# Kernel tuning notes

Measured on AMD Instinct MI355X. Metric: run time of the kernel, lower is better.

Reference implementation:

```python
import jax, jax.numpy as jnp
import numpy as np

EPS = 1e-5

def bn_relu(y, g, b):
    # BatchNorm1d in training mode: stats over (B, L) per channel, biased variance
    mu = jnp.mean(y, axis=(0, 2), keepdims=True)
    var = jnp.var(y, axis=(0, 2), keepdims=True)
    yn = (y - mu) * jax.lax.rsqrt(var + EPS)
    return jax.nn.relu(yn * g[None, :, None] + b[None, :, None])

def conv1x1_pad1(x, W):
    # Conv1d(k=1, padding=1, bias=False): pointwise matmul then zero-pad length by 1 each side
    y = jnp.einsum('bcl,oc->bol', x, W)
    return jnp.pad(y, ((0, 0), (0, 0), (1, 1)))

def conv1x1(x, W, b):
    return jnp.einsum('bcl,oc->bol', x, W) + b[None, :, None]

def conv3_pad1(x, W):
    # Conv1d(k=3, padding=1, bias=False); W: [O, C, 3]
    return jax.lax.conv_general_dilated(x, W, window_strides=(1,), padding=((1, 1),),
                                        dimension_numbers=('NCH', 'OIH', 'NCH'))

def pam(f, Wq, bq, Wk, bk, Wv, bv, gamma):
    q = conv1x1(f, Wq, bq)          # [B, C//8, L]
    k = conv1x1(f, Wk, bk)          # [B, C//8, L]
    v = conv1x1(f, Wv, bv)          # [B, C, L]
    energy = jnp.einsum('bql,bqm->blm', q, k)   # [B, L, L]
    attn = jax.nn.softmax(energy, axis=-1)
    out = jnp.einsum('bcm,blm->bcl', v, attn)
    return gamma * out + f

def cam(f, gamma):
    energy = jnp.einsum('bcl,bdl->bcd', f, f)    # [B, C, C]
    energy_new = jnp.max(energy, axis=-1, keepdims=True) - energy
    attn = jax.nn.softmax(energy_new, axis=-1)
    out = jnp.einsum('bcd,bdl->bcl', attn, f)
    return gamma * out + f

def setup_inputs() -> dict:
    key = jax.random.key(0)
    ks = jax.random.split(key, 24)
    B, C, L = 8, 256, 2046
    IC, OC = C // 4, 128  # inter_channels=64, out_channels
    s = 0.05
    d = {
        'x':   jax.random.normal(ks[0], (B, C, L), jnp.float32),
        'W5a': jax.random.normal(ks[1], (IC, C), jnp.float32) * s,
        'g5a': jnp.ones((IC,), jnp.float32), 'b5a': jnp.zeros((IC,), jnp.float32),
        'W5c': jax.random.normal(ks[2], (IC, C), jnp.float32) * s,
        'g5c': jnp.ones((IC,), jnp.float32), 'b5c': jnp.zeros((IC,), jnp.float32),
        'Wq':  jax.random.normal(ks[3], (IC // 8, IC), jnp.float32) * s,
        'bq':  jnp.zeros((IC // 8,), jnp.float32),
        'Wk':  jax.random.normal(ks[4], (IC // 8, IC), jnp.float32) * s,
        'bk':  jnp.zeros((IC // 8,), jnp.float32),
        'Wv':  jax.random.normal(ks[5], (IC, IC), jnp.float32) * s,
        'bv':  jnp.zeros((IC,), jnp.float32),
        'gamma_pam': jnp.full((1,), 0.1, jnp.float32),
        'gamma_cam': jnp.full((1,), 0.1, jnp.float32),
        'W51': jax.random.normal(ks[6], (IC, IC, 3), jnp.float32) * s,
        'g51': jnp.ones((IC,), jnp.float32), 'b51': jnp.zeros((IC,), jnp.float32),
        'W52': jax.random.normal(ks[7], (IC, IC, 3), jnp.float32) * s,
        'g52': jnp.ones((IC,), jnp.float32), 'b52': jnp.zeros((IC,), jnp.float32),
        'W6':  jax.random.normal(ks[8], (OC, IC), jnp.float32) * s,
        'b6':  jnp.zeros((OC,), jnp.float32),
        'W7':  jax.random.normal(ks[9], (OC, IC), jnp.float32) * s,
        'b7':  jnp.zeros((OC,), jnp.float32),
        'W8':  jax.random.normal(ks[10], (OC, IC), jnp.float32) * s,
        'b8':  jnp.zeros((OC,), jnp.float32),
    }
    return d

def reference(x, W5a, g5a, b5a, W5c, g5c, b5c, Wq, bq, Wk, bk, Wv, bv,
              gamma_pam, gamma_cam, W51, g51, b51, W52, g52, b52,
              W6, b6, W7, b7, W8, b8):
    # dropout (p=0.1) treated as identity (eval mode)
    feat1 = bn_relu(conv1x1_pad1(x, W5a), g5a, b5a)          # [B, IC, L+2]
    sa_feat = pam(feat1, Wq, bq, Wk, bk, Wv, bv, gamma_pam)
    sa_conv = bn_relu(conv3_pad1(sa_feat, W51), g51, b51)
    sa_output = conv1x1(sa_conv, W6, b6)                     # [B, OC, L+2]
    feat2 = bn_relu(conv1x1_pad1(x, W5c), g5c, b5c)
    sc_feat = cam(feat2, gamma_cam)
    sc_conv = bn_relu(conv3_pad1(sc_feat, W52), g52, b52)
    sc_output = conv1x1(sc_conv, W7, b7)
    feat_sum = sa_conv + sc_conv
    sasc = conv1x1(feat_sum, W8, b8)
    # pool == 'maxpool' selects AdaptiveAvgPool1d(1) in the original (note swap)
    sasc = jnp.mean(sasc, axis=-1)                            # [B, OC]
    return (sasc, sa_output, sc_output)
```

## Files before the change

### kernel.cpp

```cpp
#include <hip/hip_runtime.h>
#include <math.h>

#define B 8
#define C 256
#define L 2046
#define LP 2048
#define IC 64
#define OC 128
#define BN_EPS 1e-5f
#define INVN (1.f / 16384.f)

#define OFF_Y1T    0u
#define OFF_Y2C    524288u
#define OFF_Y51T   2097152u
#define OFF_Y52T   2621440u
#define OFF_VB     3145728u
#define OFF_QT     3670016u
#define OFF_KT     3735552u
#define OFF_EPART  3866624u
#define OFF_STATS1 4423680u
#define OFF_STATS2 4424704u
#define OFF_W5BF   4425728u
#define OFF_W67    4442112u
#define OFF_WT     4450304u
#define OFF_WQKV   4462592u
#define OFF_BQKV   4465152u

typedef __attribute__((ext_vector_type(8))) short bshort8;
typedef __attribute__((ext_vector_type(4))) float f32x4;

__device__ __forceinline__ unsigned short f2bf(float f) {
    union { float f; unsigned int u; } v; v.f = f;
    return (unsigned short)((v.u + 0x8000u) >> 16);
}
__device__ __forceinline__ float bf2f(unsigned short u) {
    union { unsigned int i; float f; } v; v.i = ((unsigned int)u) << 16;
    return v.f;
}
__device__ __forceinline__ unsigned int pk2(float a, float b) {
    union { float f; unsigned int u; } va, vb; va.f = a; vb.f = b;
    return __builtin_amdgcn_perm(vb.u + 0x8000u, va.u + 0x8000u, 0x07060302u);
}

__device__ __forceinline__ void load_coef(const float* __restrict__ STATS,
        const float* __restrict__ g, const float* __restrict__ beta,
        int base, int cnt, float* cA, float* cB, int t) {
    if (t < cnt) {
        int ch = base + t;
        float s = STATS[ch * 2] + STATS[256 + ch * 2] + STATS[512 + ch * 2] + STATS[768 + ch * 2];
        float q = STATS[ch * 2 + 1] + STATS[256 + ch * 2 + 1] + STATS[512 + ch * 2 + 1] + STATS[768 + ch * 2 + 1];
        float mu = s * INVN;
        float var = q * INVN - mu * mu;
        float A = g[t] * rsqrtf(var + BN_EPS);
        cA[t] = A;
        cB[t] = beta[t] - mu * A;
    }
}

__global__ __launch_bounds__(256) void k_wprep(
        const float* __restrict__ W5a, const float* __restrict__ W5c,
        const float* __restrict__ W6, const float* __restrict__ W7,
        const float* __restrict__ W51, const float* __restrict__ W52,
        const float* __restrict__ Wq, const float* __restrict__ Wk,
        const float* __restrict__ Wv, const float* __restrict__ bq,
        const float* __restrict__ bk, const float* __restrict__ bv,
        const float* __restrict__ b8,
        unsigned short* __restrict__ W5BF, unsigned short* __restrict__ W67,
        unsigned short* __restrict__ WT, unsigned short* __restrict__ WQKV,
        float* __restrict__ BQKV, float* __restrict__ STATS1,
        float* __restrict__ STATS2, float* __restrict__ out_sasc) {
    int i = blockIdx.x * 256 + threadIdx.x;
    if (i < 32768) {
        int o = i >> 8, c = i & 255;
        W5BF[i] = f2bf(o < 64 ? W5a[o * 256 + c] : W5c[(o - 64) * 256 + c]);
    } else if (i < 49152) {
        int j = i - 32768; int g = j >> 13; int r = j & 8191;
        W67[j] = f2bf(g ? W7[r] : W6[r]);
    } else if (i < 73728) {
        int j = i - 49152;
        int c = j & 63, o = (j >> 6) & 63, wt = j >> 12; int w = wt / 3, t = wt % 3;
        const float* Ws = w ? W52 : W51;
        WT[j] = f2bf(Ws[(o * 64 + c) * 3 + t]);
    } else if (i < 78848) {
        int j = i - 73728; int o = j >> 6, c = j & 63;
        float v = o < 8 ? Wq[o * 64 + c] : (o < 16 ? Wk[(o - 8) * 64 + c] : Wv[(o - 16) * 64 + c]);
        WQKV[j] = f2bf(v);
    } else if (i < 78928) {
        int o = i - 78848;
        BQKV[o] = o < 8 ? bq[o] : (o < 16 ? bk[o - 8] : bv[o - 16]);
    } else if (i < 80976) {
        int j = i - 78928;
        if (j < 1024) STATS1[j] = 0.f; else STATS2[j - 1024] = 0.f;
    } else if (i < 82000) {
        int j = i - 80976;
        out_sasc[j] = b8[j & 127];
    }
}

__global__ __launch_bounds__(256) void k_conv1(const float* __restrict__ x,
        const unsigned short* __restrict__ W5BF,
        unsigned short* __restrict__ Y1T, unsigned short* __restrict__ Y2C,
        float* __restrict__ STATS1) {
    __shared__ unsigned short xt[64][264];
    __shared__ float lds_part[4][64];
    int lt = blockIdx.x, b = blockIdx.y;
    int l0 = lt * 64;
    int t = threadIdx.x;
    {
        int j = t & 63, cg = t >> 6;
        int ls = l0 - 1 + j;
        bool ok = (ls >= 0) && (ls < L);
        const float* xs = x + (size_t)(b * C + cg * 64) * L + ls;
        unsigned short* row = &xt[j][cg * 64];
#pragma unroll
        for (int c8 = 0; c8 < 8; ++c8) {
            unsigned int pk[4];
#pragma unroll
            for (int i = 0; i < 4; ++i) {
                float v0 = ok ? xs[(size_t)(c8 * 8 + 2 * i) * L] : 0.f;
                float v1 = ok ? xs[(size_t)(c8 * 8 + 2 * i + 1) * L] : 0.f;
                pk[i] = pk2(v0, v1);
            }
            *(uint4*)(row + c8 * 8) = *(const uint4*)pk;
        }
    }
    __syncthreads();
    int w = t >> 6, lane = t & 63, n = lane & 15, quad = lane >> 4;
    bshort8 wf[2][8];
#pragma unroll
    for (int oi = 0; oi < 2; ++oi)
#pragma unroll
        for (int kt = 0; kt < 8; ++kt)
            wf[oi][kt] = *(const bshort8*)(W5BF + (size_t)((w * 2 + oi) * 16 + n) * C + kt * 32 + quad * 8);
    f32x4 acc[2][4];
#pragma unroll
    for (int oi = 0; oi < 2; ++oi)
#pragma unroll
        for (int sub = 0; sub < 4; ++sub) acc[oi][sub] = (f32x4){0.f, 0.f, 0.f, 0.f};
#pragma unroll
    for (int sub = 0; sub < 4; ++sub) {
        int lloc = sub * 16 + n;
#pragma unroll
        for (int kt = 0; kt < 8; ++kt) {
            bshort8 xb = *(const bshort8*)(&xt[lloc][kt * 32 + quad * 8]);
            acc[0][sub] = __builtin_amdgcn_mfma_f32_16x16x32_bf16(wf[0][kt], xb, acc[0][sub], 0, 0, 0);
            acc[1][sub] = __builtin_amdgcn_mfma_f32_16x16x32_bf16(wf[1][kt], xb, acc[1][sub], 0, 0, 0);
        }
    }
    if (w < 2) {
#pragma unroll
        for (int sub = 0; sub < 4; ++sub) {
            int lp = l0 + sub * 16 + n;
#pragma unroll
            for (int oi = 0; oi < 2; ++oi) {
                int ot = w * 2 + oi;
                uint2 pv;
                pv.x = pk2(acc[oi][sub][0], acc[oi][sub][1]);
                pv.y = pk2(acc[oi][sub][2], acc[oi][sub][3]);
                *(uint2*)(Y1T + ((size_t)(b * LP + lp)) * IC + ot * 16 + quad * 4) = pv;
            }
        }
    } else {
#pragma unroll
        for (int oi = 0; oi < 2; ++oi) {
            int ot = (w - 2) * 2 + oi;
#pragma unroll
            for (int r = 0; r < 4; ++r) {
                int o = ot * 16 + quad * 4 + r;
                unsigned short* dst = Y2C + ((size_t)(b * IC + o)) * LP + l0;
#pragma unroll
                for (int sub = 0; sub < 4; ++sub)
                    dst[sub * 16 + n] = f2bf(acc[oi][sub][r]);
            }
        }
    }
#pragma unroll
    for (int oi = 0; oi < 2; ++oi)
#pragma unroll
        for (int r = 0; r < 4; ++r) {
            float s = 0.f, q = 0.f;
#pragma unroll
            for (int sub = 0; sub < 4; ++sub) {
                float v = acc[oi][sub][r];
                s += v; q += v * v;
            }
#pragma unroll
            for (int msk = 1; msk < 16; msk <<= 1) {
                s += __shfl_xor(s, msk, 64);
                q += __shfl_xor(q, msk, 64);
            }
            if (n == 0) {
                int ci = oi * 16 + quad * 4 + r;
                lds_part[w][ci * 2] = s;
                lds_part[w][ci * 2 + 1] = q;
            }
        }
    __syncthreads();
    {
        int ch = t >> 1, wsrc = ch >> 5;
        int idx = ((ch & 31) << 1) | (t & 1);
        atomicAdd(&STATS1[(blockIdx.x & 3) * 256 + t], lds_part[wsrc][idx]);
    }
}

__device__ void role_qkv(char* dynsm, int lt, int b,
        const unsigned short* __restrict__ Y1T, const float* __restrict__ STATS1,
        const float* __restrict__ g5a, const float* __restrict__ b5a,
        const unsigned short* __restrict__ WQKV, const float* __restrict__ BQKV,
        unsigned short* __restrict__ QT, unsigned short* __restrict__ KT,
        unsigned short* __restrict__ VB) {
    float* cA = (float*)dynsm;
    float* cB = cA + 64;
    load_coef(STATS1, g5a, b5a, 0, 64, cA, cB, threadIdx.x);
    __syncthreads();
    int t = threadIdx.x;
    int w = t >> 6, lane = t & 63, n = lane & 15, quad = lane >> 4;
    int lrow = lt * 64 + w * 16 + n;
    bshort8 fb[2];
#pragma unroll
    for (int kt = 0; kt < 2; ++kt) {
        bshort8 raw = *(const bshort8*)(Y1T + ((size_t)(b * LP + lrow)) * IC + kt * 32 + quad * 8);
        bshort8 f;
#pragma unroll
        for (int j = 0; j < 8; ++j) {
            int c = kt * 32 + quad * 8 + j;
            float v = fmaxf(fmaf(cA[c], bf2f((unsigned short)raw[j]), cB[c]), 0.f);
            ((unsigned short*)&f)[j] = f2bf(v);
        }
        fb[kt] = f;
    }
    f32x4 acc[5];
#pragma unroll
    for (int ot = 0; ot < 5; ++ot) {
        f32x4 a = {0.f, 0.f, 0.f, 0.f};
#pragma unroll
        for (int kt = 0; kt < 2; ++kt) {
            bshort8 wf = *(const bshort8*)(WQKV + (size_t)(ot * 16 + n) * IC + kt * 32 + quad * 8);
            a = __builtin_amdgcn_mfma_f32_16x16x32_bf16(wf, fb[kt], a, 0, 0, 0);
        }
        acc[ot] = a;
    }
#pragma unroll
    for (int ot = 0; ot < 5; ++ot)
#pragma unroll
        for (int r = 0; r < 4; ++r) {
            int o = ot * 16 + quad * 4 + r;
            unsigned short bv16 = f2bf(acc[ot][r] + BQKV[o]);
            if (ot == 0) {
                if (o < 8) QT[((size_t)(b * LP + lrow)) * 8 + o] = bv16;
                else KT[((size_t)(b * LP + lrow)) * 8 + (o - 8)] = bv16;
            } else {
                VB[((size_t)(b * IC + (o - 16))) * LP + lrow] = bv16;
            }
        }
}

__device__ void role_gram(char* dynsm, int blk, int b,
        const unsigned short* __restrict__ Y2C, const float* __restrict__ STATS1,
        const float* __restrict__ g5c, const float* __restrict__ b5c,
        float* __restrict__ EPART) {
    float* cA = (float*)dynsm;
    float* cB = cA + 64;
    load_coef(STATS1, g5c, b5c, 64, 64, cA, cB, threadIdx.x);
    __syncthreads();
    int t = threadIdx.x;
    int w = t >> 6, lane = t & 63, n = lane & 15, quad = lane >> 4;
    f32x4 acc[4][4];
#pragma unroll
    for (int ti = 0; ti < 4; ++ti)
#pragma unroll
        for (int tj = 0; tj < 4; ++tj) acc[ti][tj] = (f32x4){0.f, 0.f, 0.f, 0.f};
    for (int chunk = 0; chunk < 4; ++chunk) {
        int lb = (blk * 4 + w) * 128 + chunk * 32 + quad * 8;
        bshort8 frag[4];
#pragma unroll
        for (int g = 0; g < 4; ++g) {
            int c = g * 16 + n;
            bshort8 raw = *(const bshort8*)(Y2C + ((size_t)(b * IC + c)) * LP + lb);
            bshort8 f;
            float A = cA[c], Bc = cB[c];
#pragma unroll
            for (int j = 0; j < 8; ++j)
                ((unsigned short*)&f)[j] = f2bf(fmaxf(fmaf(A, bf2f((unsigned short)raw[j]), Bc), 0.f));
            frag[g] = f;
        }
#pragma unroll
        for (int ti = 0; ti < 4; ++ti)
#pragma unroll
            for (int tj = 0; tj < 4; ++tj)
                acc[ti][tj] = __builtin_amdgcn_mfma_f32_16x16x32_bf16(frag[ti], frag[tj], acc[ti][tj], 0, 0, 0);
    }
    float* ep = EPART + ((size_t)(b * 16 + blk * 4 + w)) * 4096;
#pragma unroll
    for (int ti = 0; ti < 4; ++ti)
#pragma unroll
        for (int tj = 0; tj < 4; ++tj)
#pragma unroll
            for (int r = 0; r < 4; ++r)
                ep[(ti * 16 + quad * 4 + r) * 64 + tj * 16 + n] = acc[ti][tj][r];
}

__global__ __launch_bounds__(256) void k_fuse1(
        const unsigned short* __restrict__ Y1T, const unsigned short* __restrict__ Y2C,
        const float* __restrict__ STATS1,
        const float* __restrict__ g5a, const float* __restrict__ b5a,
        const float* __restrict__ g5c, const float* __restrict__ b5c,
        const unsigned short* __restrict__ WQKV, const float* __restrict__ BQKV,
        unsigned short* __restrict__ QT, unsigned short* __restrict__ KT,
        unsigned short* __restrict__ VB, float* __restrict__ EPART) {
    extern __shared__ char dynsm[];
    int idx = blockIdx.x;
    if (idx < 256) role_qkv(dynsm, idx & 31, idx >> 5, Y1T, STATS1, g5a, b5a,
                            WQKV, BQKV, QT, KT, VB);
    else { int g = idx - 256; role_gram(dynsm, g & 3, g >> 2, Y2C, STATS1, g5c, b5c, EPART); }
}

__device__ void role_pam_full(char* dynsm, int qt, int b,
        const unsigned short* __restrict__ qT, const unsigned short* __restrict__ kT,
        const unsigned short* __restrict__ vb,
        const unsigned short* __restrict__ Y1T, const float* __restrict__ STATS1,
        const float* __restrict__ g5a, const float* __restrict__ b5a,
        const float* __restrict__ gamma, const unsigned short* __restrict__ WT,
        unsigned short* __restrict__ Y51T, float* __restrict__ STATS2) {
    unsigned short* vs0 = (unsigned short*)dynsm;
    unsigned short* vs1 = vs0 + 8704;
    unsigned short* ps  = (unsigned short*)(dynsm + 34816);
    unsigned short* tile = ps;
    float* os = (float*)dynsm;
    float* cA = (float*)(dynsm + 44032);
    float* cB = cA + 64;
    float* dn = cB + 64;
    float* lds_part = dn + 64;
    int base = qt * 62 - 1;
    int tid = threadIdx.x;
    int wq = tid >> 6, lane = tid & 63, n = lane & 15, quad = lane >> 4;
    int sch = tid >> 2, skf = (tid & 3) * 32;
    load_coef(STATS1, g5a, b5a, 0, 64, cA, cB, tid);
    int qrow = base + wq * 16 + n;
    int qcl = qrow < 0 ? 0 : (qrow > LP - 1 ? LP - 1 : qrow);
    bshort8 qa = {};
    if (quad == 0)
        qa = *(const bshort8*)(qT + ((size_t)(b * LP + qcl)) * 8);
    f32x4 acc[4];
#pragma unroll
    for (int s = 0; s < 4; ++s) acc[s] = (f32x4){0.f, 0.f, 0.f, 0.f};
    float li[4] = {0.f, 0.f, 0.f, 0.f};
    unsigned short* pw = ps + wq * 16 * 72;
    const unsigned short* vsrc = vb + ((size_t)(b * IC + sch)) * LP + skf;

    {
        bshort8 v0[4];
#pragma unroll
        for (int i = 0; i < 4; ++i) v0[i] = *(const bshort8*)(vsrc + i * 8);
        unsigned short* d = vs0 + sch * 136 + skf;
#pragma unroll
        for (int i = 0; i < 4; ++i) *(bshort8*)(d + i * 8) = v0[i];
    }
    bshort8 kb[4];
#pragma unroll
    for (int s = 0; s < 4; ++s) kb[s] = (bshort8){};
    if (quad == 0) {
#pragma unroll
        for (int s = 0; s < 4; ++s)
            kb[s] = *(const bshort8*)(kT + ((size_t)(b * LP + s * 16 + n)) * 8);
    }
    __syncthreads();
    for (int sup = 0; sup < 16; ++sup) {
        unsigned short* cur = (sup & 1) ? vs1 : vs0;
        unsigned short* nxt = (sup & 1) ? vs0 : vs1;
        bshort8 vrg[4];
        if (sup < 15) {
#pragma unroll
            for (int i = 0; i < 4; ++i)
                vrg[i] = *(const bshort8*)(vsrc + (sup + 1) * 128 + i * 8);
        }
        __builtin_amdgcn_sched_barrier(0);
#pragma unroll
        for (int ki = 0; ki < 2; ++ki) {
            int g = sup * 2 + ki;
            bshort8 kn[4];
#pragma unroll
            for (int s = 0; s < 4; ++s) kn[s] = (bshort8){};
            if (g < 31 && quad == 0) {
#pragma unroll
                for (int s = 0; s < 4; ++s)
                    kn[s] = *(const bshort8*)(kT + ((size_t)(b * LP + (g + 1) * 64 + s * 16 + n)) * 8);
            }
            f32x4 sc[4];
#pragma unroll
            for (int s = 0; s < 4; ++s)
                sc[s] = __builtin_amdgcn_mfma_f32_16x16x32_bf16(qa, kb[s],
                            (f32x4){0.f, 0.f, 0.f, 0.f}, 0, 0, 0);
#pragma unroll
            for (int s = 0; s < 4; ++s)
#pragma unroll
                for (int r = 0; r < 4; ++r) {
                    float p = __expf(sc[s][r]);
                    li[r] += p;
                    pw[(quad * 4 + r) * 72 + s * 16 + n] = f2bf(p);
                }
#pragma unroll
            for (int step = 0; step < 2; ++step) {
                bshort8 pa = *(const bshort8*)(pw + n * 72 + step * 32 + quad * 8);
#pragma unroll
                for (int s = 0; s < 4; ++s) {
                    bshort8 vf = *(const bshort8*)(cur + (s * 16 + n) * 136 + ki * 64 + step * 32 + quad * 8);
                    acc[s] = __builtin_amdgcn_mfma_f32_16x16x32_bf16(pa, vf, acc[s], 0, 0, 0);
                }
            }
#pragma unroll
            for (int s = 0; s < 4; ++s) kb[s] = kn[s];
        }
        if (sup < 15) {
            unsigned short* d = nxt + sch * 136 + skf;
#pragma unroll
            for (int i = 0; i < 4; ++i) *(bshort8*)(d + i * 8) = vrg[i];
        }
        __syncthreads();
    }
#pragma unroll
    for (int s = 0; s < 4; ++s)
#pragma unroll
        for (int r = 0; r < 4; ++r)
            os[(s * 16 + n) * 65 + wq * 16 + quad * 4 + r] = acc[s][r];
#pragma unroll
    for (int r = 0; r < 4; ++r) {
        float s_ = li[r];
#pragma unroll
        for (int msk = 1; msk < 16; msk <<= 1) s_ += __shfl_xor(s_, msk, 64);
        if (n == 0) dn[wq * 16 + quad * 4 + r] = s_;
    }
    __syncthreads();
    float gm = gamma[0];
    {
        int c = tid >> 2, qc = tid & 3;
#pragma unroll
        for (int i = 0; i < 16; ++i) {
            int r = qc * 16 + i;
            int absr = base + r;
            float val = 0.f;
            if (absr >= 0 && absr < LP) {
                unsigned short raw = Y1T[((size_t)(b * LP + absr)) * IC + c];
                float f1v = fmaxf(fmaf(cA[c], bf2f(raw), cB[c]), 0.f);
                val = fmaf(gm, os[c * 65 + r] / dn[r], f1v);
            }
            tile[r * 72 + c] = f2bf(val);
        }
    }
    __syncthreads();
    {
        int j = wq * 16 + n;
        int absout = base + 1 + j;
        bool valid = (j < 62) && (absout < LP);
        f32x4 a3[4];
#pragma unroll
        for (int ot = 0; ot < 4; ++ot) a3[ot] = (f32x4){0.f, 0.f, 0.f, 0.f};
#pragma unroll
        for (int t3 = 0; t3 < 3; ++t3) {
            bshort8 fb0 = *(const bshort8*)(tile + (j + t3) * 72 + quad * 8);
            bshort8 fb1 = *(const bshort8*)(tile + (j + t3) * 72 + 32 + quad * 8);
#pragma unroll
            for (int ot = 0; ot < 4; ++ot) {
                bshort8 w0 = *(const bshort8*)(WT + ((size_t)(t3 * 64 + ot * 16 + n)) * IC + quad * 8);
                bshort8 w1 = *(const bshort8*)(WT + ((size_t)(t3 * 64 + ot * 16 + n)) * IC + 32 + quad * 8);
                a3[ot] = __builtin_amdgcn_mfma_f32_16x16x32_bf16(w0, fb0, a3[ot], 0, 0, 0);
                a3[ot] = __builtin_amdgcn_mfma_f32_16x16x32_bf16(w1, fb1, a3[ot], 0, 0, 0);
            }
        }
        if (valid) {
#pragma unroll
            for (int ot = 0; ot < 4; ++ot) {
                uint2 pv;
                pv.x = pk2(a3[ot][0], a3[ot][1]);
                pv.y = pk2(a3[ot][2], a3[ot][3]);
                *(uint2*)(Y51T + ((size_t)(b * LP + absout)) * IC + ot * 16 + quad * 4) = pv;
            }
        }
#pragma unroll
        for (int ot = 0; ot < 4; ++ot)
#pragma unroll
            for (int r = 0; r < 4; ++r) {
                float s = valid ? a3[ot][r] : 0.f;
                float q = s * s;
#pragma unroll
                for (int msk = 1; msk < 16; msk <<= 1) {
                    s += __shfl_xor(s, msk, 64);
                    q += __shfl_xor(q, msk, 64);
                }
                if (n == 0) {
                    int cch = ot * 16 + quad * 4 + r;
                    lds_part[wq * 128 + cch * 2] = s;
                    lds_part[wq * 128 + cch * 2 + 1] = q;
                }
            }
        __syncthreads();
        if (tid < 128) {
            float s = lds_part[tid] + lds_part[128 + tid] + lds_part[256 + tid] + lds_part[384 + tid];
            atomicAdd(&STATS2[(qt & 3) * 256 + tid], s);
        }
    }
}

__device__ __forceinline__ void conv3_from_tile_cam(const unsigned short* tile,
        const unsigned short* __restrict__ WT, unsigned short* __restrict__ dst,
        int b, int l0, float* lds_part, float* __restrict__ STATS2,
        int blockx, int tl) {
    int w = tl >> 6, lane = tl & 63, n = lane & 15, quad = lane >> 4;
    int lrow = l0 + w * 16 + n;
    f32x4 acc[4];
#pragma unroll
    for (int ot = 0; ot < 4; ++ot) acc[ot] = (f32x4){0.f, 0.f, 0.f, 0.f};
#pragma unroll
    for (int t3 = 0; t3 < 3; ++t3) {
        int trow = w * 16 + n + t3;
        bshort8 fb0 = *(const bshort8*)(tile + trow * 72 + quad * 8);
        bshort8 fb1 = *(const bshort8*)(tile + trow * 72 + 32 + quad * 8);
#pragma unroll
        for (int ot = 0; ot < 4; ++ot) {
            bshort8 w0 = *(const bshort8*)(WT + ((size_t)(t3 * 64 + ot * 16 + n)) * IC + quad * 8);
            bshort8 w1 = *(const bshort8*)(WT + ((size_t)(t3 * 64 + ot * 16 + n)) * IC + 32 + quad * 8);
            acc[ot] = __builtin_amdgcn_mfma_f32_16x16x32_bf16(w0, fb0, acc[ot], 0, 0, 0);
            acc[ot] = __builtin_amdgcn_mfma_f32_16x16x32_bf16(w1, fb1, acc[ot], 0, 0, 0);
        }
    }
#pragma unroll
    for (int ot = 0; ot < 4; ++ot) {
        uint2 pv;
        pv.x = pk2(acc[ot][0], acc[ot][1]);
        pv.y = pk2(acc[ot][2], acc[ot][3]);
        *(uint2*)(dst + ((size_t)(b * LP + lrow)) * IC + ot * 16 + quad * 4) = pv;
    }
#pragma unroll
    for (int ot = 0; ot < 4; ++ot)
#pragma unroll
        for (int r = 0; r < 4; ++r) {
            float s = acc[ot][r], q = s * s;
#pragma unroll
            for (int msk = 1; msk < 16; msk <<= 1) {
                s += __shfl_xor(s, msk, 64);
                q += __shfl_xor(q, msk, 64);
            }
            if (n == 0) {
                int cch = ot * 16 + quad * 4 + r;
                lds_part[w * 128 + cch * 2] = s;
                lds_part[w * 128 + cch * 2 + 1] = q;
            }
        }
    __syncthreads();
    if (tl < 128) {
        float s = lds_part[tl] + lds_part[128 + tl] + lds_part[256 + tl] + lds_part[384 + tl];
        atomicAdd(&STATS2[(blockx & 3) * 256 + 128 + tl], s);
    }
}

__device__ void role_cam_full(char* sm, int tl, int lt, int b,
        const float* __restrict__ EPART, const unsigned short* __restrict__ Y2C,
        const float* __restrict__ STATS1,
        const float* __restrict__ g5c, const float* __restrict__ b5c,
        const float* __restrict__ gamma, const unsigned short* __restrict__ WT,
        unsigned short* __restrict__ Y52T, float* __restrict__ STATS2) {
    float* as = (float*)sm;
    float* cA = as + 4096; float* cB = cA + 64;
    unsigned short* tile = (unsigned short*)(cB + 64);
    float* lds_part = (float*)(tile + 4752);
    int l0 = lt * 64;
    load_coef(STATS1, g5c, b5c, 64, 64, cA, cB, tl);
    for (int idx = tl; idx < 4096; idx += 256) {
        float s = 0.f;
#pragma unroll
        for (int ch = 0; ch < 16; ++ch) s += EPART[((size_t)(b * 16 + ch)) * 4096 + idx];
        as[idx] = s;
    }
    __syncthreads();
    {
        int row = tl >> 2, qd = tl & 3;
        float v[16];
#pragma unroll
        for (int i = 0; i < 16; ++i) v[i] = as[row * 64 + qd * 16 + i];
        float mn = v[0];
#pragma unroll
        for (int i = 1; i < 16; ++i) mn = fminf(mn, v[i]);
        mn = fminf(mn, __shfl_xor(mn, 1, 64));
        mn = fminf(mn, __shfl_xor(mn, 2, 64));
        float s = 0.f;
#pragma unroll
        for (int i = 0; i < 16; ++i) { v[i] = __expf(mn - v[i]); s += v[i]; }
        s += __shfl_xor(s, 1, 64);
        s += __shfl_xor(s, 2, 64);
        float inv = 1.f / s;
#pragma unroll
        for (int i = 0; i < 16; ++i) as[row * 64 + qd * 16 + i] = v[i] * inv;
    }
    __syncthreads();
    float gm = gamma[0];
    {
        int lq = tl & 63, cg = tl >> 6;
        const unsigned short* fb = Y2C + (size_t)b * IC * LP + l0 + lq;
        float acc[16];
#pragma unroll
        for (int i = 0; i < 16; ++i) acc[i] = 0.f;
        for (int d4 = 0; d4 < 16; ++d4) {
            float fv[4];
#pragma unroll
            for (int i = 0; i < 4; ++i) {
                int d = 4 * d4 + i;
                fv[i] = fmaxf(fmaf(cA[d], bf2f(fb[(size_t)d * LP]), cB[d]), 0.f);
            }
#pragma unroll
            for (int cc = 0; cc < 16; ++cc) {
                const float4 a4 = *reinterpret_cast<const float4*>(as + (cg * 16 + cc) * 64 + d4 * 4);
                acc[cc] += a4.x * fv[0] + a4.y * fv[1] + a4.z * fv[2] + a4.w * fv[3];
            }
        }
#pragma unroll
        for (int cc = 0; cc < 16; ++cc) {
            int c = cg * 16 + cc;
            float res = fmaxf(fmaf(cA[c], bf2f(fb[(size_t)c * LP]), cB[c]), 0.f);
            tile[(1 + lq) * 72 + c] = f2bf(fmaf(gm, acc[cc], res));
        }
    }
    float* fcol = lds_part;
    if (tl < 128) {
        int row = tl >> 6;
        int ch = tl & 63;
        int l = l0 - 1 + row * 65;
        float v = 0.f;
        if (l >= 0 && l < LP)
            v = fmaxf(fmaf(cA[ch], bf2f(Y2C[(size_t)b * IC * LP + (size_t)ch * LP + l]), cB[ch]), 0.f);
        fcol[row * 64 + ch] = v;
    }
    __syncthreads();
    if (tl < 128) {
        int sel = tl & 1;
        int row = sel ? 65 : 0;
        int ch = tl >> 1;
        int l = l0 - 1 + (sel ? 65 : 0);
        float val = 0.f;
        if (l >= 0 && l < LP) {
            const float* fc = fcol + sel * 64;
            float a = 0.f;
#pragma unroll 8
            for (int d = 0; d < 64; ++d) a = fmaf(as[ch * 64 + d], fc[d], a);
            val = fmaf(gm, a, fc[ch]);
        }
        tile[row * 72 + ch] = f2bf(val);
    }
    __syncthreads();
    conv3_from_tile_cam(tile, WT, Y52T, b, l0, lds_part, STATS2, lt, tl);
}

__global__ __launch_bounds__(256) void k_fuse2(
        const unsigned short* __restrict__ QT, const unsigned short* __restrict__ KT,
        const unsigned short* __restrict__ VB,
        const unsigned short* __restrict__ Y1T, const unsigned short* __restrict__ Y2C,
        const float* __restrict__ STATS1,
        const float* __restrict__ g5a, const float* __restrict__ b5a,
        const float* __restrict__ g5c, const float* __restrict__ b5c,
        const float* __restrict__ gpam, const float* __restrict__ gcam,
        const float* __restrict__ EPART, const unsigned short* __restrict__ WTall,
        unsigned short* __restrict__ Y51T, unsigned short* __restrict__ Y52T,
        float* __restrict__ STATS2) {
    extern __shared__ char dynsm[];
    int idx = blockIdx.x;
    if (idx < 272) {
        int b = idx / 34; int qt = idx - b * 34;
        role_pam_full(dynsm, qt, b, QT, KT, VB, Y1T, STATS1, g5a, b5a, gpam,
                      WTall, Y51T, STATS2);
    } else {
        int g = idx - 272;
        role_cam_full(dynsm, threadIdx.x, g & 31, g >> 5, EPART, Y2C, STATS1,
                      g5c, b5c, gcam, WTall + 12288, Y52T, STATS2);
    }
}

__global__ __launch_bounds__(256) void k_final(const unsigned short* __restrict__ Y51T,
        const unsigned short* __restrict__ Y52T, const float* __restrict__ STATS2,
        const float* __restrict__ g51, const float* __restrict__ b51,
        const float* __restrict__ g52, const float* __restrict__ b52,
        const unsigned short* __restrict__ W67,
        const float* __restrict__ b6, const float* __restrict__ b7,
        const float* __restrict__ W8,
        float* __restrict__ out_sa, float* __restrict__ out_sc,
        float* __restrict__ out_sasc) {
    __shared__ float cA[128], cB[128];
    __shared__ float fsw[4][64];
    __shared__ float chsum[64];
    int lt = blockIdx.x, og = blockIdx.y, b = blockIdx.z;
    int t = threadIdx.x;
    if (t < 128) {
        float s = STATS2[t * 2] + STATS2[256 + t * 2] + STATS2[512 + t * 2] + STATS2[768 + t * 2];
        float q = STATS2[t * 2 + 1] + STATS2[256 + t * 2 + 1] + STATS2[512 + t * 2 + 1] + STATS2[768 + t * 2 + 1];
        float mu = s * INVN, var = q * INVN - mu * mu;
        float gv = t < 64 ? g51[t] : g52[t - 64];
        float bv = t < 64 ? b51[t] : b52[t - 64];
        float A = gv * rsqrtf(var + BN_EPS);
        cA[t] = A; cB[t] = bv - mu * A;
    }
    __syncthreads();
    int w = t >> 6, lane = t & 63, n = lane & 15, quad = lane >> 4;
    int lrow = lt * 64 + w * 16 + n;
    float fs_lane[16];
    bshort8 ba[2], bb[2];
#pragma unroll
    for (int kt = 0; kt < 2; ++kt) {
        bshort8 ra = *(const bshort8*)(Y51T + ((size_t)(b * LP + lrow)) * IC + kt * 32 + quad * 8);
        bshort8 rb = *(const bshort8*)(Y52T + ((size_t)(b * LP + lrow)) * IC + kt * 32 + quad * 8);
        bshort8 fa, fb;
#pragma unroll
        for (int j = 0; j < 8; ++j) {
            int c = kt * 32 + quad * 8 + j;
            float v1 = fmaxf(fmaf(cA[c], bf2f((unsigned short)ra[j]), cB[c]), 0.f);
            float v2 = fmaxf(fmaf(cA[64 + c], bf2f((unsigned short)rb[j]), cB[64 + c]), 0.f);
            ((unsigned short*)&fa)[j] = f2bf(v1);
            ((unsigned short*)&fb)[j] = f2bf(v2);
            fs_lane[kt * 8 + j] = v1 + v2;
        }
        ba[kt] = fa; bb[kt] = fb;
    }
    f32x4 accA[4], accB[4];
#pragma unroll
    for (int ot = 0; ot < 4; ++ot) {
        accA[ot] = (f32x4){0.f, 0.f, 0.f, 0.f};
        accB[ot] = (f32x4){0.f, 0.f, 0.f, 0.f};
    }
#pragma unroll
    for (int ot = 0; ot < 4; ++ot)
#pragma unroll
        for (int kt = 0; kt < 2; ++kt) {
            bshort8 wa = *(const bshort8*)(W67 + (size_t)(og * 64 + ot * 16 + n) * IC + kt * 32 + quad * 8);
            bshort8 wb = *(const bshort8*)(W67 + 8192 + (size_t)(og * 64 + ot * 16 + n) * IC + kt * 32 + quad * 8);
            accA[ot] = __builtin_amdgcn_mfma_f32_16x16x32_bf16(wa, ba[kt], accA[ot], 0, 0, 0);
            accB[ot] = __builtin_amdgcn_mfma_f32_16x16x32_bf16(wb, bb[kt], accB[ot], 0, 0, 0);
        }
#pragma unroll
    for (int ot = 0; ot < 4; ++ot)
#pragma unroll
        for (int r = 0; r < 4; ++r) {
            int o = og * 64 + ot * 16 + quad * 4 + r;
            out_sa[((size_t)(b * OC + o)) * LP + lrow] = accA[ot][r] + b6[o];
            out_sc[((size_t)(b * OC + o)) * LP + lrow] = accB[ot][r] + b7[o];
        }
    if (og == 0) {
#pragma unroll
        for (int i = 0; i < 16; ++i) {
            float s = fs_lane[i];
#pragma unroll
            for (int msk = 1; msk < 16; msk <<= 1) s += __shfl_xor(s, msk, 64);
            if (n == 0) {
                int c = (i >> 3) * 32 + quad * 8 + (i & 7);
                fsw[w][c] = s;
            }
        }
        __syncthreads();
        if (t < 64) chsum[t] = fsw[0][t] + fsw[1][t] + fsw[2][t] + fsw[3][t];
        __syncthreads();
        if (t < 128) {
            float s = 0.f;
            for (int c = 0; c < 64; ++c) s = fmaf(W8[t * 64 + c], chsum[c], s);
            atomicAdd(&out_sasc[b * OC + t], s * (1.f / (float)LP));
        }
    }
}

extern "C" void kernel_launch(void* const* d_in, const int* in_sizes, int n_in,
                              void* d_out, int out_size, void* d_ws, size_t ws_size,
                              hipStream_t stream) {
    (void)in_sizes; (void)n_in; (void)out_size; (void)ws_size;
    const float* x    = (const float*)d_in[0];
    const float* W5a  = (const float*)d_in[1];
    const float* g5a  = (const float*)d_in[2];
    const float* b5a  = (const float*)d_in[3];
    const float* W5c  = (const float*)d_in[4];
    const float* g5c  = (const float*)d_in[5];
    const float* b5c  = (const float*)d_in[6];
    const float* Wq   = (const float*)d_in[7];
    const float* bq   = (const float*)d_in[8];
    const float* Wk   = (const float*)d_in[9];
    const float* bk   = (const float*)d_in[10];
    const float* Wv   = (const float*)d_in[11];
    const float* bv   = (const float*)d_in[12];
    const float* gpam = (const float*)d_in[13];
    const float* gcam = (const float*)d_in[14];
    const float* W51  = (const float*)d_in[15];
    const float* g51  = (const float*)d_in[16];
    const float* b51  = (const float*)d_in[17];
    const float* W52  = (const float*)d_in[18];
    const float* g52  = (const float*)d_in[19];
    const float* b52  = (const float*)d_in[20];
    const float* W6   = (const float*)d_in[21];
    const float* b6   = (const float*)d_in[22];
    const float* W7   = (const float*)d_in[23];
    const float* b7   = (const float*)d_in[24];
    const float* W8   = (const float*)d_in[25];
    const float* b8   = (const float*)d_in[26];

    float* ws = (float*)d_ws;
    float* out = (float*)d_out;
    unsigned short* Y1T  = (unsigned short*)(ws + OFF_Y1T);
    unsigned short* Y2C  = (unsigned short*)(ws + OFF_Y2C);
    unsigned short* Y51T = (unsigned short*)(ws + OFF_Y51T);
    unsigned short* Y52T = (unsigned short*)(ws + OFF_Y52T);
    unsigned short* VB   = (unsigned short*)(ws + OFF_VB);
    unsigned short* QT   = (unsigned short*)(ws + OFF_QT);
    unsigned short* KT   = (unsigned short*)(ws + OFF_KT);
    float* EPART  = ws + OFF_EPART;
    float* STATS1 = ws + OFF_STATS1;
    float* STATS2 = ws + OFF_STATS2;
    unsigned short* W5BF = (unsigned short*)(ws + OFF_W5BF);
    unsigned short* W67  = (unsigned short*)(ws + OFF_W67);
    unsigned short* WT   = (unsigned short*)(ws + OFF_WT);
    unsigned short* WQKV = (unsigned short*)(ws + OFF_WQKV);
    float* BQKV = ws + OFF_BQKV;

    float* out_sa = out + B * OC;
    float* out_sc = out + B * OC + (size_t)B * OC * LP;

    k_wprep<<<321, 256, 0, stream>>>(W5a, W5c, W6, W7, W51, W52, Wq, Wk, Wv,
                                     bq, bk, bv, b8, W5BF, W67, WT, WQKV, BQKV,
                                     STATS1, STATS2, out);
    k_conv1<<<dim3(32, B), 256, 0, stream>>>(x, W5BF, Y1T, Y2C, STATS1);
    k_fuse1<<<288, 256, 512, stream>>>(Y1T, Y2C, STATS1, g5a, b5a, g5c, b5c,
                                       WQKV, BQKV, QT, KT, VB, EPART);
    k_fuse2<<<528, 256, 46848, stream>>>(QT, KT, VB, Y1T, Y2C, STATS1,
                                         g5a, b5a, g5c, b5c, gpam, gcam,
                                         EPART, WT, Y51T, Y52T, STATS2);
    k_final<<<dim3(32, 2, B), 256, 0, stream>>>(Y51T, Y52T, STATS2, g51, b51, g52, b52,
                                                W67, b6, b7, W8, out_sa, out_sc, out);
}
```

Before: 212.3 us.

## Software-pipeline PAM attention: overlap QK MFMA of next sub-tile with softmax of current

Restructures the PAM inner loop so each 128-key super-step issues the second half's QK^T MFMAs before the first half's PV MFMAs, with the P buffer double-buffered per wave (pw0/pw1). K fragments for both halves and the next step are preloaded at the top of the step. s_setprio hints raise priority around the MFMA bursts. The goal is to hide exp/LDS-write latency behind matrix work. In exchange it uses more LDS (46848 to 56064 bytes dynamic) and more registers, which may reduce occupancy.

```diff
diff --git a/kernel.cpp b/kernel.cpp
--- a/kernel.cpp
+++ b/kernel.cpp
@@ -327,7 +327,7 @@
     unsigned short* ps  = (unsigned short*)(dynsm + 34816);
     unsigned short* tile = ps;
     float* os = (float*)dynsm;
-    float* cA = (float*)(dynsm + 44032);
+    float* cA = (float*)(dynsm + 53248);
     float* cB = cA + 64;
     float* dn = cB + 64;
     float* lds_part = dn + 64;
@@ -345,7 +345,8 @@
 #pragma unroll
     for (int s = 0; s < 4; ++s) acc[s] = (f32x4){0.f, 0.f, 0.f, 0.f};
     float li[4] = {0.f, 0.f, 0.f, 0.f};
-    unsigned short* pw = ps + wq * 16 * 72;
+    unsigned short* pw0 = ps + wq * 2304;
+    unsigned short* pw1 = pw0 + 1152;
     const unsigned short* vsrc = vb + ((size_t)(b * IC + sch)) * LP + skf;
 
     {
@@ -374,49 +375,78 @@
             for (int i = 0; i < 4; ++i)
                 vrg[i] = *(const bshort8*)(vsrc + (sup + 1) * 128 + i * 8);
         }
+        bshort8 kb1[4], kn[4];
+#pragma unroll
+        for (int s = 0; s < 4; ++s) { kb1[s] = (bshort8){}; kn[s] = (bshort8){}; }
+        if (quad == 0) {
+            int m1 = sup * 128 + 64;
+#pragma unroll
+            for (int s = 0; s < 4; ++s)
+                kb1[s] = *(const bshort8*)(kT + ((size_t)(b * LP + m1 + s * 16 + n)) * 8);
+            if (sup < 15) {
+#pragma unroll
+                for (int s = 0; s < 4; ++s)
+                    kn[s] = *(const bshort8*)(kT + ((size_t)(b * LP + m1 + 64 + s * 16 + n)) * 8);
+            }
+        }
         __builtin_amdgcn_sched_barrier(0);
-#pragma unroll
-        for (int ki = 0; ki < 2; ++ki) {
-            int g = sup * 2 + ki;
-            bshort8 kn[4];
-#pragma unroll
-            for (int s = 0; s < 4; ++s) kn[s] = (bshort8){};
-            if (g < 31 && quad == 0) {
-#pragma unroll
-                for (int s = 0; s < 4; ++s)
-                    kn[s] = *(const bshort8*)(kT + ((size_t)(b * LP + (g + 1) * 64 + s * 16 + n)) * 8);
-            }
-            f32x4 sc[4];
-#pragma unroll
-            for (int s = 0; s < 4; ++s)
-                sc[s] = __builtin_amdgcn_mfma_f32_16x16x32_bf16(qa, kb[s],
-                            (f32x4){0.f, 0.f, 0.f, 0.f}, 0, 0, 0);
-#pragma unroll
-            for (int s = 0; s < 4; ++s)
-#pragma unroll
-                for (int r = 0; r < 4; ++r) {
-                    float p = __expf(sc[s][r]);
-                    li[r] += p;
-                    pw[(quad * 4 + r) * 72 + s * 16 + n] = f2bf(p);
-                }
-#pragma unroll
-            for (int step = 0; step < 2; ++step) {
-                bshort8 pa = *(const bshort8*)(pw + n * 72 + step * 32 + quad * 8);
-#pragma unroll
-                for (int s = 0; s < 4; ++s) {
-                    bshort8 vf = *(const bshort8*)(cur + (s * 16 + n) * 136 + ki * 64 + step * 32 + quad * 8);
-                    acc[s] = __builtin_amdgcn_mfma_f32_16x16x32_bf16(pa, vf, acc[s], 0, 0, 0);
-                }
-            }
-#pragma unroll
-            for (int s = 0; s < 4; ++s) kb[s] = kn[s];
-        }
+        f32x4 sc0[4], sc1[4];
+        __builtin_amdgcn_s_setprio(1);
+#pragma unroll
+        for (int s = 0; s < 4; ++s)
+            sc0[s] = __builtin_amdgcn_mfma_f32_16x16x32_bf16(qa, kb[s],
+                        (f32x4){0.f, 0.f, 0.f, 0.f}, 0, 0, 0);
+        __builtin_amdgcn_s_setprio(0);
+#pragma unroll
+        for (int s = 0; s < 4; ++s)
+#pragma unroll
+            for (int r = 0; r < 4; ++r) {
+                float p = __expf(sc0[s][r]);
+                li[r] += p;
+                pw0[(quad * 4 + r) * 72 + s * 16 + n] = f2bf(p);
+            }
+        __builtin_amdgcn_s_setprio(1);
+#pragma unroll
+        for (int s = 0; s < 4; ++s)
+            sc1[s] = __builtin_amdgcn_mfma_f32_16x16x32_bf16(qa, kb1[s],
+                        (f32x4){0.f, 0.f, 0.f, 0.f}, 0, 0, 0);
+#pragma unroll
+        for (int step = 0; step < 2; ++step) {
+            bshort8 pa = *(const bshort8*)(pw0 + n * 72 + step * 32 + quad * 8);
+#pragma unroll
+            for (int s = 0; s < 4; ++s) {
+                bshort8 vf = *(const bshort8*)(cur + (s * 16 + n) * 136 + step * 32 + quad * 8);
+                acc[s] = __builtin_amdgcn_mfma_f32_16x16x32_bf16(pa, vf, acc[s], 0, 0, 0);
+            }
+        }
+        __builtin_amdgcn_s_setprio(0);
+#pragma unroll
+        for (int s = 0; s < 4; ++s)
+#pragma unroll
+            for (int r = 0; r < 4; ++r) {
+                float p = __expf(sc1[s][r]);
+                li[r] += p;
+                pw1[(quad * 4 + r) * 72 + s * 16 + n] = f2bf(p);
+            }
+        __builtin_amdgcn_s_setprio(1);
+#pragma unroll
+        for (int step = 0; step < 2; ++step) {
+            bshort8 pa = *(const bshort8*)(pw1 + n * 72 + step * 32 + quad * 8);
+#pragma unroll
+            for (int s = 0; s < 4; ++s) {
+                bshort8 vf = *(const bshort8*)(cur + (s * 16 + n) * 136 + 64 + step * 32 + quad * 8);
+                acc[s] = __builtin_amdgcn_mfma_f32_16x16x32_bf16(pa, vf, acc[s], 0, 0, 0);
+            }
+        }
+        __builtin_amdgcn_s_setprio(0);
         if (sup < 15) {
             unsigned short* d = nxt + sch * 136 + skf;
 #pragma unroll
             for (int i = 0; i < 4; ++i) *(bshort8*)(d + i * 8) = vrg[i];
         }
         __syncthreads();
+#pragma unroll
+        for (int s = 0; s < 4; ++s) kb[s] = kn[s];
     }
 #pragma unroll
     for (int s = 0; s < 4; ++s)
@@ -821,7 +851,7 @@
     k_conv1<<<dim3(32, B), 256, 0, stream>>>(x, W5BF, Y1T, Y2C, STATS1);
     k_fuse1<<<288, 256, 512, stream>>>(Y1T, Y2C, STATS1, g5a, b5a, g5c, b5c,
                                        WQKV, BQKV, QT, KT, VB, EPART);
-    k_fuse2<<<528, 256, 46848, stream>>>(QT, KT, VB, Y1T, Y2C, STATS1,
+    k_fuse2<<<528, 256, 56064, stream>>>(QT, KT, VB, Y1T, Y2C, STATS1,
                                          g5a, b5a, g5c, b5c, gpam, gcam,
                                          EPART, WT, Y51T, Y52T, STATS2);
     k_final<<<dim3(32, 2, B), 256, 0, stream>>>(Y51T, Y52T, STATS2, g51, b51, g52, b52,
```

Measured after the change: 215.4 us. Within noise of the previous version (+1.4%).

## Split PAM attention key range across two blocks with atomic-ticket merge

Applied to the files above, without the earlier changes.

Each PAM query tile is now handled by two blocks, each covering half of the key/value length. Each block writes its partial output and softmax denominators to a workspace buffer. An atomic ticket picks the last-finishing block, which merges both halves and runs the rest of the fused epilogue. This doubles the PAM block count to improve occupancy and shorten the serial key loop, at the cost of extra global traffic, a fence and an atomic, and a reliance on a fixed exp without a running max being additive across the halves.

```diff
diff --git a/kernel.cpp b/kernel.cpp
--- a/kernel.cpp
+++ b/kernel.cpp
@@ -25,6 +25,8 @@
 #define OFF_WT     4450304u
 #define OFF_WQKV   4462592u
 #define OFF_BQKV   4465152u
+#define OFF_TICK   4466688u
+#define OFF_OP2    4467200u
 
 typedef __attribute__((ext_vector_type(8))) short bshort8;
 typedef __attribute__((ext_vector_type(4))) float f32x4;
@@ -68,7 +70,8 @@
         unsigned short* __restrict__ W5BF, unsigned short* __restrict__ W67,
         unsigned short* __restrict__ WT, unsigned short* __restrict__ WQKV,
         float* __restrict__ BQKV, float* __restrict__ STATS1,
-        float* __restrict__ STATS2, float* __restrict__ out_sasc) {
+        float* __restrict__ STATS2, float* __restrict__ out_sasc,
+        int* __restrict__ TICK) {
     int i = blockIdx.x * 256 + threadIdx.x;
     if (i < 32768) {
         int o = i >> 8, c = i & 255;
@@ -94,6 +97,8 @@
     } else if (i < 82000) {
         int j = i - 80976;
         out_sasc[j] = b8[j & 127];
+    } else if (i < 82272) {
+        TICK[i - 82000] = 0;
     }
 }
 
@@ -315,13 +320,14 @@
     else { int g = idx - 256; role_gram(dynsm, g & 3, g >> 2, Y2C, STATS1, g5c, b5c, EPART); }
 }
 
-__device__ void role_pam_full(char* dynsm, int qt, int b,
+__device__ void role_pam_full(char* dynsm, int p, int h, int qt, int b,
         const unsigned short* __restrict__ qT, const unsigned short* __restrict__ kT,
         const unsigned short* __restrict__ vb,
         const unsigned short* __restrict__ Y1T, const float* __restrict__ STATS1,
         const float* __restrict__ g5a, const float* __restrict__ b5a,
         const float* __restrict__ gamma, const unsigned short* __restrict__ WT,
-        unsigned short* __restrict__ Y51T, float* __restrict__ STATS2) {
+        unsigned short* __restrict__ Y51T, float* __restrict__ STATS2,
+        float* __restrict__ OP2, int* __restrict__ TICK) {
     unsigned short* vs0 = (unsigned short*)dynsm;
     unsigned short* vs1 = vs0 + 8704;
     unsigned short* ps  = (unsigned short*)(dynsm + 34816);
@@ -332,6 +338,7 @@
     float* dn = cB + 64;
     float* lds_part = dn + 64;
     int base = qt * 62 - 1;
+    int hbase = h * 1024;
     int tid = threadIdx.x;
     int wq = tid >> 6, lane = tid & 63, n = lane & 15, quad = lane >> 4;
     int sch = tid >> 2, skf = (tid & 3) * 32;
@@ -346,7 +353,7 @@
     for (int s = 0; s < 4; ++s) acc[s] = (f32x4){0.f, 0.f, 0.f, 0.f};
     float li[4] = {0.f, 0.f, 0.f, 0.f};
     unsigned short* pw = ps + wq * 16 * 72;
-    const unsigned short* vsrc = vb + ((size_t)(b * IC + sch)) * LP + skf;
+    const unsigned short* vsrc = vb + ((size_t)(b * IC + sch)) * LP + hbase + skf;
 
     {
         bshort8 v0[4];
@@ -362,14 +369,14 @@
     if (quad == 0) {
 #pragma unroll
         for (int s = 0; s < 4; ++s)
-            kb[s] = *(const bshort8*)(kT + ((size_t)(b * LP + s * 16 + n)) * 8);
-    }
-    __syncthreads();
-    for (int sup = 0; sup < 16; ++sup) {
+            kb[s] = *(const bshort8*)(kT + ((size_t)(b * LP + hbase + s * 16 + n)) * 8);
+    }
+    __syncthreads();
+    for (int sup = 0; sup < 8; ++sup) {
         unsigned short* cur = (sup & 1) ? vs1 : vs0;
         unsigned short* nxt = (sup & 1) ? vs0 : vs1;
         bshort8 vrg[4];
-        if (sup < 15) {
+        if (sup < 7) {
 #pragma unroll
             for (int i = 0; i < 4; ++i)
                 vrg[i] = *(const bshort8*)(vsrc + (sup + 1) * 128 + i * 8);
@@ -381,10 +388,10 @@
             bshort8 kn[4];
 #pragma unroll
             for (int s = 0; s < 4; ++s) kn[s] = (bshort8){};
-            if (g < 31 && quad == 0) {
+            if (g < 15 && quad == 0) {
 #pragma unroll
                 for (int s = 0; s < 4; ++s)
-                    kn[s] = *(const bshort8*)(kT + ((size_t)(b * LP + (g + 1) * 64 + s * 16 + n)) * 8);
+                    kn[s] = *(const bshort8*)(kT + ((size_t)(b * LP + hbase + (g + 1) * 64 + s * 16 + n)) * 8);
             }
             f32x4 sc[4];
 #pragma unroll
@@ -395,9 +402,9 @@
             for (int s = 0; s < 4; ++s)
 #pragma unroll
                 for (int r = 0; r < 4; ++r) {
-                    float p = __expf(sc[s][r]);
-                    li[r] += p;
-                    pw[(quad * 4 + r) * 72 + s * 16 + n] = f2bf(p);
+                    float pv = __expf(sc[s][r]);
+                    li[r] += pv;
+                    pw[(quad * 4 + r) * 72 + s * 16 + n] = f2bf(pv);
                 }
 #pragma unroll
             for (int step = 0; step < 2; ++step) {
@@ -411,7 +418,7 @@
 #pragma unroll
             for (int s = 0; s < 4; ++s) kb[s] = kn[s];
         }
-        if (sup < 15) {
+        if (sup < 7) {
             unsigned short* d = nxt + sch * 136 + skf;
 #pragma unroll
             for (int i = 0; i < 4; ++i) *(bshort8*)(d + i * 8) = vrg[i];
@@ -430,6 +437,24 @@
         for (int msk = 1; msk < 16; msk <<= 1) s_ += __shfl_xor(s_, msk, 64);
         if (n == 0) dn[wq * 16 + quad * 4 + r] = s_;
     }
+    __syncthreads();
+    {
+        float* dst = OP2 + (size_t)(p * 2 + h) * 4160;
+        int c = tid >> 2, qc = tid & 3;
+#pragma unroll
+        for (int i = 0; i < 16; ++i)
+            dst[c * 64 + qc * 16 + i] = os[c * 65 + qc * 16 + i];
+        if (tid < 64) dst[4096 + tid] = dn[tid];
+    }
+    __syncthreads();
+    if (tid == 0) {
+        __threadfence();
+        ((int*)lds_part)[0] = atomicAdd(TICK + p, 1);
+    }
+    __syncthreads();
+    if (((int*)lds_part)[0] == 0) return;
+    const float* oth = OP2 + (size_t)(p * 2 + (1 - h)) * 4160;
+    if (tid < 64) dn[tid] += oth[4096 + tid];
     __syncthreads();
     float gm = gamma[0];
     {
@@ -438,11 +463,12 @@
         for (int i = 0; i < 16; ++i) {
             int r = qc * 16 + i;
             int absr = base + r;
+            float o2 = os[c * 65 + r] + oth[c * 64 + r];
             float val = 0.f;
             if (absr >= 0 && absr < LP) {
                 unsigned short raw = Y1T[((size_t)(b * LP + absr)) * IC + c];
                 float f1v = fmaxf(fmaf(cA[c], bf2f(raw), cB[c]), 0.f);
-                val = fmaf(gm, os[c * 65 + r] / dn[r], f1v);
+                val = fmaf(gm, o2 / dn[r], f1v);
             }
             tile[r * 72 + c] = f2bf(val);
         }
@@ -659,15 +685,17 @@
         const float* __restrict__ gpam, const float* __restrict__ gcam,
         const float* __restrict__ EPART, const unsigned short* __restrict__ WTall,
         unsigned short* __restrict__ Y51T, unsigned short* __restrict__ Y52T,
-        float* __restrict__ STATS2) {
+        float* __restrict__ STATS2, float* __restrict__ OP2,
+        int* __restrict__ TICK) {
     extern __shared__ char dynsm[];
     int idx = blockIdx.x;
-    if (idx < 272) {
-        int b = idx / 34; int qt = idx - b * 34;
-        role_pam_full(dynsm, qt, b, QT, KT, VB, Y1T, STATS1, g5a, b5a, gpam,
-                      WTall, Y51T, STATS2);
+    if (idx < 544) {
+        int p = idx >> 1, h = idx & 1;
+        int b = p / 34; int qt = p - b * 34;
+        role_pam_full(dynsm, p, h, qt, b, QT, KT, VB, Y1T, STATS1, g5a, b5a,
+                      gpam, WTall, Y51T, STATS2, OP2, TICK);
     } else {
-        int g = idx - 272;
+        int g = idx - 544;
         role_cam_full(dynsm, threadIdx.x, g & 31, g >> 5, EPART, Y2C, STATS1,
                       g5c, b5c, gcam, WTall + 12288, Y52T, STATS2);
     }
@@ -811,19 +839,22 @@
     unsigned short* WT   = (unsigned short*)(ws + OFF_WT);
     unsigned short* WQKV = (unsigned short*)(ws + OFF_WQKV);
     float* BQKV = ws + OFF_BQKV;
+    int*   TICK = (int*)(ws + OFF_TICK);
+    float* OP2  = ws + OFF_OP2;
 
     float* out_sa = out + B * OC;
     float* out_sc = out + B * OC + (size_t)B * OC * LP;
 
-    k_wprep<<<321, 256, 0, stream>>>(W5a, W5c, W6, W7, W51, W52, Wq, Wk, Wv,
+    k_wprep<<<322, 256, 0, stream>>>(W5a, W5c, W6, W7, W51, W52, Wq, Wk, Wv,
                                      bq, bk, bv, b8, W5BF, W67, WT, WQKV, BQKV,
-                                     STATS1, STATS2, out);
+                                     STATS1, STATS2, out, TICK);
     k_conv1<<<dim3(32, B), 256, 0, stream>>>(x, W5BF, Y1T, Y2C, STATS1);
     k_fuse1<<<288, 256, 512, stream>>>(Y1T, Y2C, STATS1, g5a, b5a, g5c, b5c,
                                        WQKV, BQKV, QT, KT, VB, EPART);
-    k_fuse2<<<528, 256, 46848, stream>>>(QT, KT, VB, Y1T, Y2C, STATS1,
+    k_fuse2<<<800, 256, 46848, stream>>>(QT, KT, VB, Y1T, Y2C, STATS1,
                                          g5a, b5a, g5c, b5c, gpam, gcam,
-                                         EPART, WT, Y51T, Y52T, STATS2);
+                                         EPART, WT, Y51T, Y52T, STATS2,
+                                         OP2, TICK);
     k_final<<<dim3(32, 2, B), 256, 0, stream>>>(Y51T, Y52T, STATS2, g51, b51, g52, b52,
                                                 W67, b6, b7, W8, out_sa, out_sc, out);
 }
```

Measured after the change: 232.8 us. 1.1x slower.
